# Performance work log

Measured on AMD Instinct MI355X. Metric: run time of the kernel, lower is better.

Reference implementation:

```python
import jax, jax.numpy as jnp
import numpy as np

B_BATCH = 16384   # number of independent control queries (timesteps/trials)
P = 32            # observation dim p = C.shape[0]
MC = 16           # control dim m_control = B.shape[1]
H = 24            # h (== h_tilde in the module, since it sets self.h_tilde = h)
M = 64            # m (== m_tilde, since the module sets self.m_tilde = m)
L = M + M + 1     # history length needed: max delay is j+k = m_tilde + m - 1


def setup_inputs() -> dict:
    key = jax.random.key(0)
    ks = jax.random.split(key, 9)
    return {
        # y_rev[b, d, :] == y_nat_history[-d-1] (most-recent-first reversed history)
        "y_rev": jax.random.normal(ks[0], (B_BATCH, L, P), dtype=jnp.float32),
        "M0": jax.random.normal(ks[1], (MC, P), dtype=jnp.float32),
        "M_tilde": jax.random.normal(ks[2], (H, MC, P), dtype=jnp.float32),
        "M_0l": jax.random.normal(ks[3], (H, MC, P), dtype=jnp.float32),
        "M_big": jax.random.normal(ks[4], (H, H, MC, P), dtype=jnp.float32),
        # eigenvalues of the PSD Hankel matrices: positive
        "sigma": jax.random.uniform(ks[5], (H,), dtype=jnp.float32, minval=0.01, maxval=1.0),
        "lambda_e": jax.random.uniform(ks[6], (H,), dtype=jnp.float32, minval=0.01, maxval=1.0),
        "phi": jax.random.normal(ks[7], (M, H), dtype=jnp.float32),
        "phi_tilde": jax.random.normal(ks[8], (M, H), dtype=jnp.float32),
    }


def reference(y_rev, M0, M_tilde, M_0l, M_big, sigma, lambda_e, phi, phi_tilde):
    # Term 1: M_0 @ y_t  -> [B, MC]
    u = jnp.einsum("cp,bp->bc", M0, y_rev[:, 0])

    # Term 2: sum_{i,j>=1} lambda_i^{1/4} phi_tilde[j-1,i] (M_tilde[i] @ y_{t-j})
    pt = phi_tilde * (lambda_e ** 0.25)[None, :]            # [M, H] (j-1, i)
    T2 = jnp.einsum("ji,icp->jcp", pt, M_tilde)             # [M, MC, P]
    u = u + jnp.einsum("jcp,bjp->bc", T2, y_rev[:, 1:M + 1])

    # Term 3: sum_{l,k>=0} sigma_l^{1/4} phi[k,l] (M_0l[l] @ y_{t-k})
    ps = phi * (sigma ** 0.25)[None, :]                     # [M, H] (k, l)
    T3 = jnp.einsum("kl,lcp->kcp", ps, M_0l)                # [M, MC, P]
    u = u + jnp.einsum("kcp,bkp->bc", T3, y_rev[:, 0:M])

    # Term 4: sum_{i,j,l,k} (sigma_l lambda_i)^{1/4} phi[k,l] phi_tilde[j-1,i] (M[i][l] @ y_{t-j-k})
    # Collapse (j,k) into delay d=j+k via 1-D convolution per (i,l):
    #   conv(phi_tilde[:,i], phi[:,l])[n] corresponds to delay d = n+1.
    conv = jax.vmap(jax.vmap(jnp.convolve, in_axes=(None, 1)), in_axes=(1, None))
    W4 = conv(phi_tilde, phi)                               # [H(i), H(l), 2M-1]
    scale = (lambda_e[:, None] * sigma[None, :]) ** 0.25    # [H(i), H(l)]
    T4 = jnp.einsum("ild,ilcp->dcp", W4 * scale[:, :, None], M_big)  # [2M-1, MC, P]
    u = u + jnp.einsum("dcp,bdp->bc", T4, y_rev[:, 1:2 * M])

    return u  # [B, MC]
```

## Files before the change

### kernel.cpp

```cpp
#include <hip/hip_runtime.h>
#include <hip/hip_bf16.h>

#define BB    16384
#define PP    32
#define MCC   16
#define HH    24
#define MM    64
#define LL    129
#define YROW  (LL*PP)
#define KK    (128*PP)

#define ROWS   64
#define TPB    512
#define STAGES 16
#define SK     256
#define SROWSTRIDE 265

__device__ __forceinline__ float rl(float v, int lane) {
    return __int_as_float(__builtin_amdgcn_readlane(__float_as_int(v), lane));
}

__global__ __launch_bounds__(256) void setup_k(
    const float* __restrict__ M0,  const float* __restrict__ Mt,
    const float* __restrict__ M0l, const float* __restrict__ Mb,
    const float* __restrict__ sig, const float* __restrict__ lam,
    const float* __restrict__ phi, const float* __restrict__ phit,
    float* __restrict__ Wk)
{
    __shared__ float sA[MM*HH];
    __shared__ float sB[MM*HH];
    __shared__ float sWd[HH*HH];

    const int t = threadIdx.x;
    const int d = blockIdx.x >> 1;
    const int h = blockIdx.x & 1;

#pragma unroll
    for (int r = 0; r < 6; ++r) {
        int e = t + r*256;
        int col = e % HH;
        sA[e] = phit[e] * sqrtf(sqrtf(lam[col]));
        sB[e] = phi[e]  * sqrtf(sqrtf(sig[col]));
    }
    __syncthreads();

    if (d >= 1) {
        const int n  = d - 1;
        const int lo = n > 63 ? n - 63 : 0;
        const int hi = n < 63 ? n : 63;
        for (int e = t; e < HH*HH; e += 256) {
            int i = e / HH, l = e % HH;
            float s = 0.f;
            for (int j = lo; j <= hi; ++j) s += sA[j*HH + i] * sB[(n - j)*HH + l];
            sWd[e] = s;
        }
    }
    __syncthreads();

    const int c = h*8 + (t >> 5);
    const int p = t & 31;
    float wv = 0.f;
    if (d == 0) wv += M0[c*PP + p];
    if (d >= 1 && d <= MM) {
        const int j = d - 1;
#pragma unroll
        for (int i = 0; i < HH; ++i) wv += sA[j*HH + i] * Mt[(i*MCC + c)*PP + p];
    }
    if (d < MM) {
#pragma unroll
        for (int l = 0; l < HH; ++l) wv += sB[d*HH + l] * M0l[(l*MCC + c)*PP + p];
    }
    if (d >= 1) {
        const float* mb = Mb + h*256 + t;
#pragma unroll 16
        for (int e = 0; e < HH*HH; ++e) wv += sWd[e] * mb[e*512];
    }
    Wk[(d*PP + p)*MCC + c] = wv;
}

__global__ __launch_bounds__(512) void main_k(
    const float* __restrict__ Y, const float* __restrict__ Wk,
    float* __restrict__ out)
{
    __shared__ float sY[ROWS * SROWSTRIDE];

    const int t    = threadIdx.x;
    const int w    = t >> 6;
    const int lane = t & 63;
    const int blk  = blockIdx.x;

    const int srow = t >> 3, kq = t & 7;
    const float* yst = Y + (size_t)(blk*ROWS + srow)*YROW + kq*32;
    const int wbase = srow*SROWSTRIDE + kq*33;

    const int rbase = lane*SROWSTRIDE + w*33;

    const float* wst = Wk + ((w*32 + (lane & 31))*MCC + ((lane >> 5) & 1)*8);

    float acc[16];
#pragma unroll
    for (int c = 0; c < 16; ++c) acc[c] = 0.f;

    float4 Yr[8], Wn0, Wn1, Wc0, Wc1;
#pragma unroll
    for (int i = 0; i < 8; ++i) Yr[i] = *(const float4*)(yst + 4*i);
    Wn0 = *(const float4*)(wst + 0);
    Wn1 = *(const float4*)(wst + 4);

#pragma unroll 1
    for (int s = 0; s < STAGES; ++s) {
        __syncthreads();
#pragma unroll
        for (int i = 0; i < 8; ++i) {
            int a = wbase + 4*i;
            sY[a + 0] = Yr[i].x; sY[a + 1] = Yr[i].y;
            sY[a + 2] = Yr[i].z; sY[a + 3] = Yr[i].w;
        }
        __syncthreads();

        Wc0 = Wn0; Wc1 = Wn1;
        if (s < STAGES - 1) {
            const float* yp = yst + (s + 1)*SK;
#pragma unroll
            for (int i = 0; i < 8; ++i) Yr[i] = *(const float4*)(yp + 4*i);
            const float* wp = wst + (s + 1)*SK*MCC;
            Wn0 = *(const float4*)(wp + 0);
            Wn1 = *(const float4*)(wp + 4);
        }

#pragma unroll
        for (int j = 0; j < 32; ++j) {
            float yv = sY[rbase + j];
            acc[0]  = fmaf(rl(Wc0.x, j     ), yv, acc[0]);
            acc[1]  = fmaf(rl(Wc0.y, j     ), yv, acc[1]);
            acc[2]  = fmaf(rl(Wc0.z, j     ), yv, acc[2]);
            acc[3]  = fmaf(rl(Wc0.w, j     ), yv, acc[3]);
            acc[4]  = fmaf(rl(Wc1.x, j     ), yv, acc[4]);
            acc[5]  = fmaf(rl(Wc1.y, j     ), yv, acc[5]);
            acc[6]  = fmaf(rl(Wc1.z, j     ), yv, acc[6]);
            acc[7]  = fmaf(rl(Wc1.w, j     ), yv, acc[7]);
            acc[8]  = fmaf(rl(Wc0.x, j + 32), yv, acc[8]);
            acc[9]  = fmaf(rl(Wc0.y, j + 32), yv, acc[9]);
            acc[10] = fmaf(rl(Wc0.z, j + 32), yv, acc[10]);
            acc[11] = fmaf(rl(Wc0.w, j + 32), yv, acc[11]);
            acc[12] = fmaf(rl(Wc1.x, j + 32), yv, acc[12]);
            acc[13] = fmaf(rl(Wc1.y, j + 32), yv, acc[13]);
            acc[14] = fmaf(rl(Wc1.z, j + 32), yv, acc[14]);
            acc[15] = fmaf(rl(Wc1.w, j + 32), yv, acc[15]);
        }
    }

    __syncthreads();
    float* red = sY;
#pragma unroll
    for (int c = 0; c < 16; ++c) red[t*16 + c] = acc[c];
    __syncthreads();

    if (t < 256) {
        const int row = t >> 2, c4 = t & 3;
        float4 sum = make_float4(0.f, 0.f, 0.f, 0.f);
#pragma unroll
        for (int ww = 0; ww < 8; ++ww) {
            const float* rp = &red[(ww*64 + row)*16 + c4*4];
            sum.x += rp[0]; sum.y += rp[1]; sum.z += rp[2]; sum.w += rp[3];
        }
        *(float4*)(out + (size_t)(blk*ROWS + row)*MCC + c4*4) = sum;
    }
}

extern "C" void kernel_launch(void* const* d_in, const int* in_sizes, int n_in,
                              void* d_out, int out_size, void* d_ws, size_t ws_size,
                              hipStream_t stream) {
    (void)in_sizes; (void)n_in; (void)out_size; (void)ws_size;
    const float* y    = (const float*)d_in[0];
    const float* M0   = (const float*)d_in[1];
    const float* Mt   = (const float*)d_in[2];
    const float* M0l  = (const float*)d_in[3];
    const float* Mb   = (const float*)d_in[4];
    const float* sig  = (const float*)d_in[5];
    const float* lam  = (const float*)d_in[6];
    const float* phi  = (const float*)d_in[7];
    const float* phit = (const float*)d_in[8];

    float* Wk  = (float*)d_ws;
    float* out = (float*)d_out;

    setup_k<<<256, 256, 0, stream>>>(M0, Mt, M0l, Mb, sig, lam, phi, phit, Wk);
    main_k<<<256, TPB, 0, stream>>>(y, Wk, out);
}
```

Measured before the change: 420.1 us.

## Split the K dimension across two blocks per row group and add a reduce pass

The main kernel now splits the 4096-long reduction dimension into two halves, launching 512 blocks instead of 256 so more of the GPU's compute units get work. Each half writes partial sums to the output or to a workspace buffer, and a small extra kernel adds them together. Launch bounds now request 4 blocks per multiprocessor. The cost is one extra kernel launch and an extra pass over the output, and the split path is only taken when the workspace is large enough.

```diff
diff --git a/kernel.cpp b/kernel.cpp
--- a/kernel.cpp
+++ b/kernel.cpp
@@ -9,10 +9,10 @@
 #define LL    129
 #define YROW  (LL*PP)
 #define KK    (128*PP)
+#define KHALF 2048
 
 #define ROWS   64
 #define TPB    512
-#define STAGES 16
 #define SK     256
 #define SROWSTRIDE 265
 
@@ -78,9 +78,10 @@
     Wk[(d*PP + p)*MCC + c] = wv;
 }
 
-__global__ __launch_bounds__(512) void main_k(
+template<int NSTAGES>
+__global__ __launch_bounds__(512, 4) void main_k(
     const float* __restrict__ Y, const float* __restrict__ Wk,
-    float* __restrict__ out)
+    float* __restrict__ out0, float* __restrict__ out1)
 {
     __shared__ float sY[ROWS * SROWSTRIDE];
 
@@ -88,14 +89,17 @@
     const int w    = t >> 6;
     const int lane = t & 63;
     const int blk  = blockIdx.x;
+    const int rowg = blk & 255;
+    const int kh   = blk >> 8;
 
     const int srow = t >> 3, kq = t & 7;
-    const float* yst = Y + (size_t)(blk*ROWS + srow)*YROW + kq*32;
+    const float* yst = Y + (size_t)(rowg*ROWS + srow)*YROW + kh*KHALF + kq*32;
     const int wbase = srow*SROWSTRIDE + kq*33;
 
     const int rbase = lane*SROWSTRIDE + w*33;
 
-    const float* wst = Wk + ((w*32 + (lane & 31))*MCC + ((lane >> 5) & 1)*8);
+    const float* wst = Wk + (size_t)kh*KHALF*MCC
+                         + ((w*32 + (lane & 31))*MCC + ((lane >> 5) & 1)*8);
 
     float acc[16];
 #pragma unroll
@@ -108,7 +112,7 @@
     Wn1 = *(const float4*)(wst + 4);
 
 #pragma unroll 1
-    for (int s = 0; s < STAGES; ++s) {
+    for (int s = 0; s < NSTAGES; ++s) {
         __syncthreads();
 #pragma unroll
         for (int i = 0; i < 8; ++i) {
@@ -119,7 +123,7 @@
         __syncthreads();
 
         Wc0 = Wn0; Wc1 = Wn1;
-        if (s < STAGES - 1) {
+        if (s < NSTAGES - 1) {
             const float* yp = yst + (s + 1)*SK;
 #pragma unroll
             for (int i = 0; i < 8; ++i) Yr[i] = *(const float4*)(yp + 4*i);
@@ -164,14 +168,25 @@
             const float* rp = &red[(ww*64 + row)*16 + c4*4];
             sum.x += rp[0]; sum.y += rp[1]; sum.z += rp[2]; sum.w += rp[3];
         }
-        *(float4*)(out + (size_t)(blk*ROWS + row)*MCC + c4*4) = sum;
-    }
+        float* dst = kh ? out1 : out0;
+        *(float4*)(dst + (size_t)(rowg*ROWS + row)*MCC + c4*4) = sum;
+    }
+}
+
+__global__ __launch_bounds__(256) void reduce_k(
+    const float* __restrict__ part, float* __restrict__ out)
+{
+    const int i = blockIdx.x*256 + threadIdx.x;
+    float4 a = ((float4*)out)[i];
+    float4 b = ((const float4*)part)[i];
+    a.x += b.x; a.y += b.y; a.z += b.z; a.w += b.w;
+    ((float4*)out)[i] = a;
 }
 
 extern "C" void kernel_launch(void* const* d_in, const int* in_sizes, int n_in,
                               void* d_out, int out_size, void* d_ws, size_t ws_size,
                               hipStream_t stream) {
-    (void)in_sizes; (void)n_in; (void)out_size; (void)ws_size;
+    (void)in_sizes; (void)n_in; (void)out_size;
     const float* y    = (const float*)d_in[0];
     const float* M0   = (const float*)d_in[1];
     const float* Mt   = (const float*)d_in[2];
@@ -185,6 +200,16 @@
     float* Wk  = (float*)d_ws;
     float* out = (float*)d_out;
 
+    const size_t wk_bytes   = (size_t)KK*MCC*sizeof(float);
+    const size_t part_bytes = (size_t)BB*MCC*sizeof(float);
+
     setup_k<<<256, 256, 0, stream>>>(M0, Mt, M0l, Mb, sig, lam, phi, phit, Wk);
-    main_k<<<256, TPB, 0, stream>>>(y, Wk, out);
-}
+
+    if (ws_size >= wk_bytes + part_bytes) {
+        float* part = Wk + (size_t)KK*MCC;
+        main_k<8><<<512, TPB, 0, stream>>>(y, Wk, out, part);
+        reduce_k<<<256, 256, 0, stream>>>(part, out);
+    } else {
+        main_k<16><<<256, TPB, 0, stream>>>(y, Wk, out, out);
+    }
+}
```

Result: slower. 430.6 us (+2.5%).

## Replace LDS-staged readlane GEMV with per-thread direct dot products

Applied to the files above, without the earlier changes.

The main kernel no longer stages Y through shared memory or broadcasts weights with readlane. Each thread now computes one (row, control) output as a 4096-length dot product, reading Y and a transposed weight row straight from global memory with double-buffered float4 loads. The weight layout in setup_k is transposed to be contiguous per control channel to support this. The 16 threads sharing a row re-read the same Y data through cache instead of shared memory, which removes the barriers and readlane work but raises cache and global traffic, and the final cross-warp reduction disappears.

```diff
diff --git a/kernel.cpp b/kernel.cpp
--- a/kernel.cpp
+++ b/kernel.cpp
@@ -1,5 +1,4 @@
 #include <hip/hip_runtime.h>
-#include <hip/hip_bf16.h>
 
 #define BB    16384
 #define PP    32
@@ -10,22 +9,12 @@
 #define YROW  (LL*PP)
 #define KK    (128*PP)
 
-#define ROWS   64
-#define TPB    512
-#define STAGES 16
-#define SK     256
-#define SROWSTRIDE 265
-
-__device__ __forceinline__ float rl(float v, int lane) {
-    return __int_as_float(__builtin_amdgcn_readlane(__float_as_int(v), lane));
-}
-
 __global__ __launch_bounds__(256) void setup_k(
     const float* __restrict__ M0,  const float* __restrict__ Mt,
     const float* __restrict__ M0l, const float* __restrict__ Mb,
     const float* __restrict__ sig, const float* __restrict__ lam,
     const float* __restrict__ phi, const float* __restrict__ phit,
-    float* __restrict__ Wk)
+    float* __restrict__ Wt)
 {
     __shared__ float sA[MM*HH];
     __shared__ float sB[MM*HH];
@@ -75,97 +64,47 @@
 #pragma unroll 16
         for (int e = 0; e < HH*HH; ++e) wv += sWd[e] * mb[e*512];
     }
-    Wk[(d*PP + p)*MCC + c] = wv;
+    Wt[(size_t)c*KK + d*PP + p] = wv;
 }
 
-__global__ __launch_bounds__(512) void main_k(
-    const float* __restrict__ Y, const float* __restrict__ Wk,
+#define LD(Y0,Y1,Y2,Y3,W0,W1,W2,W3,off)                                     \
+    Y0 = *(const float4*)(yp + (off));      W0 = *(const float4*)(wp + (off));      \
+    Y1 = *(const float4*)(yp + (off) + 4);  W1 = *(const float4*)(wp + (off) + 4);  \
+    Y2 = *(const float4*)(yp + (off) + 8);  W2 = *(const float4*)(wp + (off) + 8);  \
+    Y3 = *(const float4*)(yp + (off) + 12); W3 = *(const float4*)(wp + (off) + 12);
+
+#define FMA4(Yv,Wv)                                                         \
+    a0 = fmaf((Yv).x, (Wv).x, a0); a1 = fmaf((Yv).y, (Wv).y, a1);           \
+    a2 = fmaf((Yv).z, (Wv).z, a2); a3 = fmaf((Yv).w, (Wv).w, a3);
+
+__global__ __launch_bounds__(256, 4) void main_k(
+    const float* __restrict__ Y, const float* __restrict__ Wt,
     float* __restrict__ out)
 {
-    __shared__ float sY[ROWS * SROWSTRIDE];
+    const int t   = threadIdx.x;
+    const int c   = t & 15;
+    const int row = blockIdx.x * 16 + (t >> 4);
 
-    const int t    = threadIdx.x;
-    const int w    = t >> 6;
-    const int lane = t & 63;
-    const int blk  = blockIdx.x;
+    const float* yp = Y  + (size_t)row * YROW;
+    const float* wp = Wt + (size_t)c * KK;
 
-    const int srow = t >> 3, kq = t & 7;
-    const float* yst = Y + (size_t)(blk*ROWS + srow)*YROW + kq*32;
-    const int wbase = srow*SROWSTRIDE + kq*33;
+    float a0 = 0.f, a1 = 0.f, a2 = 0.f, a3 = 0.f;
+    float4 ya0, ya1, ya2, ya3, wa0, wa1, wa2, wa3;
+    float4 yb0, yb1, yb2, yb3, wb0, wb1, wb2, wb3;
 
-    const int rbase = lane*SROWSTRIDE + w*33;
-
-    const float* wst = Wk + ((w*32 + (lane & 31))*MCC + ((lane >> 5) & 1)*8);
-
-    float acc[16];
-#pragma unroll
-    for (int c = 0; c < 16; ++c) acc[c] = 0.f;
-
-    float4 Yr[8], Wn0, Wn1, Wc0, Wc1;
-#pragma unroll
-    for (int i = 0; i < 8; ++i) Yr[i] = *(const float4*)(yst + 4*i);
-    Wn0 = *(const float4*)(wst + 0);
-    Wn1 = *(const float4*)(wst + 4);
+    LD(ya0, ya1, ya2, ya3, wa0, wa1, wa2, wa3, 0)
 
 #pragma unroll 1
-    for (int s = 0; s < STAGES; ++s) {
-        __syncthreads();
-#pragma unroll
-        for (int i = 0; i < 8; ++i) {
-            int a = wbase + 4*i;
-            sY[a + 0] = Yr[i].x; sY[a + 1] = Yr[i].y;
-            sY[a + 2] = Yr[i].z; sY[a + 3] = Yr[i].w;
+    for (int q = 0; q < KK; q += 32) {
+        LD(yb0, yb1, yb2, yb3, wb0, wb1, wb2, wb3, q + 16)
+        FMA4(ya0, wa0) FMA4(ya1, wa1) FMA4(ya2, wa2) FMA4(ya3, wa3)
+        if (q + 32 < KK) {
+            LD(ya0, ya1, ya2, ya3, wa0, wa1, wa2, wa3, q + 32)
         }
-        __syncthreads();
-
-        Wc0 = Wn0; Wc1 = Wn1;
-        if (s < STAGES - 1) {
-            const float* yp = yst + (s + 1)*SK;
-#pragma unroll
-            for (int i = 0; i < 8; ++i) Yr[i] = *(const float4*)(yp + 4*i);
-            const float* wp = wst + (s + 1)*SK*MCC;
-            Wn0 = *(const float4*)(wp + 0);
-            Wn1 = *(const float4*)(wp + 4);
-        }
-
-#pragma unroll
-        for (int j = 0; j < 32; ++j) {
-            float yv = sY[rbase + j];
-            acc[0]  = fmaf(rl(Wc0.x, j     ), yv, acc[0]);
-            acc[1]  = fmaf(rl(Wc0.y, j     ), yv, acc[1]);
-            acc[2]  = fmaf(rl(Wc0.z, j     ), yv, acc[2]);
-            acc[3]  = fmaf(rl(Wc0.w, j     ), yv, acc[3]);
-            acc[4]  = fmaf(rl(Wc1.x, j     ), yv, acc[4]);
-            acc[5]  = fmaf(rl(Wc1.y, j     ), yv, acc[5]);
-            acc[6]  = fmaf(rl(Wc1.z, j     ), yv, acc[6]);
-            acc[7]  = fmaf(rl(Wc1.w, j     ), yv, acc[7]);
-            acc[8]  = fmaf(rl(Wc0.x, j + 32), yv, acc[8]);
-            acc[9]  = fmaf(rl(Wc0.y, j + 32), yv, acc[9]);
-            acc[10] = fmaf(rl(Wc0.z, j + 32), yv, acc[10]);
-            acc[11] = fmaf(rl(Wc0.w, j + 32), yv, acc[11]);
-            acc[12] = fmaf(rl(Wc1.x, j + 32), yv, acc[12]);
-            acc[13] = fmaf(rl(Wc1.y, j + 32), yv, acc[13]);
-            acc[14] = fmaf(rl(Wc1.z, j + 32), yv, acc[14]);
-            acc[15] = fmaf(rl(Wc1.w, j + 32), yv, acc[15]);
-        }
+        FMA4(yb0, wb0) FMA4(yb1, wb1) FMA4(yb2, wb2) FMA4(yb3, wb3)
     }
 
-    __syncthreads();
-    float* red = sY;
-#pragma unroll
-    for (int c = 0; c < 16; ++c) red[t*16 + c] = acc[c];
-    __syncthreads();
-
-    if (t < 256) {
-        const int row = t >> 2, c4 = t & 3;
-        float4 sum = make_float4(0.f, 0.f, 0.f, 0.f);
-#pragma unroll
-        for (int ww = 0; ww < 8; ++ww) {
-            const float* rp = &red[(ww*64 + row)*16 + c4*4];
-            sum.x += rp[0]; sum.y += rp[1]; sum.z += rp[2]; sum.w += rp[3];
-        }
-        *(float4*)(out + (size_t)(blk*ROWS + row)*MCC + c4*4) = sum;
-    }
+    out[(size_t)row * MCC + c] = (a0 + a1) + (a2 + a3);
 }
 
 extern "C" void kernel_launch(void* const* d_in, const int* in_sizes, int n_in,
@@ -182,9 +121,9 @@
     const float* phi  = (const float*)d_in[7];
     const float* phit = (const float*)d_in[8];
 
-    float* Wk  = (float*)d_ws;
+    float* Wt  = (float*)d_ws;
     float* out = (float*)d_out;
 
-    setup_k<<<256, 256, 0, stream>>>(M0, Mt, M0l, Mb, sig, lam, phi, phit, Wk);
-    main_k<<<256, TPB, 0, stream>>>(y, Wk, out);
+    setup_k<<<256, 256, 0, stream>>>(M0, Mt, M0l, Mb, sig, lam, phi, phit, Wt);
+    main_k<<<1024, 256, 0, stream>>>(y, Wt, out);
 }
```

Result: slower. 870.3 us (+107.2%).

## Double-buffer LDS tiles with XOR swizzle and halve stage size

Applied to the files above, without the earlier changes.

The main kernel now splits K into 32 stages of 128 instead of 16 stages of 256. Shared memory is double-buffered as float4 with an XOR swizzle instead of padded scalar rows, so only one barrier per stage is needed and reads are vectorized 128-bit LDS loads. The weight fragment per lane shrinks to one float4, and readlane indices are remapped to cover 16 columns per group of four. This targets barrier stalls and scalar LDS traffic, at the cost of more loop iterations and a reworked index mapping that must stay correct.

```diff
diff --git a/kernel.cpp b/kernel.cpp
--- a/kernel.cpp
+++ b/kernel.cpp
@@ -1,5 +1,4 @@
 #include <hip/hip_runtime.h>
-#include <hip/hip_bf16.h>
 
 #define BB    16384
 #define PP    32
@@ -12,9 +11,9 @@
 
 #define ROWS   64
 #define TPB    512
-#define STAGES 16
-#define SK     256
-#define SROWSTRIDE 265
+#define STAGES 32
+#define SK     128
+#define BUFF   (ROWS*SK/4)
 
 __device__ __forceinline__ float rl(float v, int lane) {
     return __int_as_float(__builtin_amdgcn_readlane(__float_as_int(v), lane));
@@ -78,11 +77,29 @@
     Wk[(d*PP + p)*MCC + c] = wv;
 }
 
+#define FMASTEP(YV, J)                                                       \
+    acc[0]  = fmaf(rl(Wc.x, (J)     ), (YV), acc[0]);                        \
+    acc[1]  = fmaf(rl(Wc.y, (J)     ), (YV), acc[1]);                        \
+    acc[2]  = fmaf(rl(Wc.z, (J)     ), (YV), acc[2]);                        \
+    acc[3]  = fmaf(rl(Wc.w, (J)     ), (YV), acc[3]);                        \
+    acc[4]  = fmaf(rl(Wc.x, (J) + 16), (YV), acc[4]);                        \
+    acc[5]  = fmaf(rl(Wc.y, (J) + 16), (YV), acc[5]);                        \
+    acc[6]  = fmaf(rl(Wc.z, (J) + 16), (YV), acc[6]);                        \
+    acc[7]  = fmaf(rl(Wc.w, (J) + 16), (YV), acc[7]);                        \
+    acc[8]  = fmaf(rl(Wc.x, (J) + 32), (YV), acc[8]);                        \
+    acc[9]  = fmaf(rl(Wc.y, (J) + 32), (YV), acc[9]);                        \
+    acc[10] = fmaf(rl(Wc.z, (J) + 32), (YV), acc[10]);                       \
+    acc[11] = fmaf(rl(Wc.w, (J) + 32), (YV), acc[11]);                       \
+    acc[12] = fmaf(rl(Wc.x, (J) + 48), (YV), acc[12]);                       \
+    acc[13] = fmaf(rl(Wc.y, (J) + 48), (YV), acc[13]);                       \
+    acc[14] = fmaf(rl(Wc.z, (J) + 48), (YV), acc[14]);                       \
+    acc[15] = fmaf(rl(Wc.w, (J) + 48), (YV), acc[15]);
+
 __global__ __launch_bounds__(512) void main_k(
     const float* __restrict__ Y, const float* __restrict__ Wk,
     float* __restrict__ out)
 {
-    __shared__ float sY[ROWS * SROWSTRIDE];
+    __shared__ float4 sY[2*BUFF];
 
     const int t    = threadIdx.x;
     const int w    = t >> 6;
@@ -90,68 +107,61 @@
     const int blk  = blockIdx.x;
 
     const int srow = t >> 3, kq = t & 7;
-    const float* yst = Y + (size_t)(blk*ROWS + srow)*YROW + kq*32;
-    const int wbase = srow*SROWSTRIDE + kq*33;
-
-    const int rbase = lane*SROWSTRIDE + w*33;
-
-    const float* wst = Wk + ((w*32 + (lane & 31))*MCC + ((lane >> 5) & 1)*8);
+    const float* yst = Y + (size_t)(blk*ROWS + srow)*YROW + kq*16;
+    const int wx = srow*32;
+    const int sx = srow & 7;
+
+    const int rbase4 = lane*32;
+    const int rx     = lane & 7;
+
+    const float* wst = Wk + ((w*16 + (lane & 15))*MCC + (lane >> 4)*4);
 
     float acc[16];
 #pragma unroll
     for (int c = 0; c < 16; ++c) acc[c] = 0.f;
 
-    float4 Yr[8], Wn0, Wn1, Wc0, Wc1;
-#pragma unroll
-    for (int i = 0; i < 8; ++i) Yr[i] = *(const float4*)(yst + 4*i);
-    Wn0 = *(const float4*)(wst + 0);
-    Wn1 = *(const float4*)(wst + 4);
+    float4 Yr[4], Wn, Wc;
+#pragma unroll
+    for (int i = 0; i < 4; ++i) Yr[i] = *(const float4*)(yst + 4*i);
+    Wn = *(const float4*)(wst);
+#pragma unroll
+    for (int i = 0; i < 4; ++i)
+        sY[wx + ((kq*4 + i) ^ sx)] = Yr[i];
 
 #pragma unroll 1
     for (int s = 0; s < STAGES; ++s) {
-        __syncthreads();
-#pragma unroll
-        for (int i = 0; i < 8; ++i) {
-            int a = wbase + 4*i;
-            sY[a + 0] = Yr[i].x; sY[a + 1] = Yr[i].y;
-            sY[a + 2] = Yr[i].z; sY[a + 3] = Yr[i].w;
-        }
-        __syncthreads();
-
-        Wc0 = Wn0; Wc1 = Wn1;
+        const int cur = s & 1;
+
+        Wc = Wn;
         if (s < STAGES - 1) {
             const float* yp = yst + (s + 1)*SK;
 #pragma unroll
-            for (int i = 0; i < 8; ++i) Yr[i] = *(const float4*)(yp + 4*i);
-            const float* wp = wst + (s + 1)*SK*MCC;
-            Wn0 = *(const float4*)(wp + 0);
-            Wn1 = *(const float4*)(wp + 4);
-        }
-
-#pragma unroll
-        for (int j = 0; j < 32; ++j) {
-            float yv = sY[rbase + j];
-            acc[0]  = fmaf(rl(Wc0.x, j     ), yv, acc[0]);
-            acc[1]  = fmaf(rl(Wc0.y, j     ), yv, acc[1]);
-            acc[2]  = fmaf(rl(Wc0.z, j     ), yv, acc[2]);
-            acc[3]  = fmaf(rl(Wc0.w, j     ), yv, acc[3]);
-            acc[4]  = fmaf(rl(Wc1.x, j     ), yv, acc[4]);
-            acc[5]  = fmaf(rl(Wc1.y, j     ), yv, acc[5]);
-            acc[6]  = fmaf(rl(Wc1.z, j     ), yv, acc[6]);
-            acc[7]  = fmaf(rl(Wc1.w, j     ), yv, acc[7]);
-            acc[8]  = fmaf(rl(Wc0.x, j + 32), yv, acc[8]);
-            acc[9]  = fmaf(rl(Wc0.y, j + 32), yv, acc[9]);
-            acc[10] = fmaf(rl(Wc0.z, j + 32), yv, acc[10]);
-            acc[11] = fmaf(rl(Wc0.w, j + 32), yv, acc[11]);
-            acc[12] = fmaf(rl(Wc1.x, j + 32), yv, acc[12]);
-            acc[13] = fmaf(rl(Wc1.y, j + 32), yv, acc[13]);
-            acc[14] = fmaf(rl(Wc1.z, j + 32), yv, acc[14]);
-            acc[15] = fmaf(rl(Wc1.w, j + 32), yv, acc[15]);
-        }
-    }
-
-    __syncthreads();
-    float* red = sY;
+            for (int i = 0; i < 4; ++i) Yr[i] = *(const float4*)(yp + 4*i);
+            Wn = *(const float4*)(wst + (size_t)(s + 1)*SK*MCC);
+        }
+
+        __syncthreads();
+
+        const float4* yb = &sY[cur*BUFF];
+#pragma unroll
+        for (int j4 = 0; j4 < 4; ++j4) {
+            float4 y4 = yb[rbase4 + ((w*4 + j4) ^ rx)];
+            FMASTEP(y4.x, j4*4 + 0)
+            FMASTEP(y4.y, j4*4 + 1)
+            FMASTEP(y4.z, j4*4 + 2)
+            FMASTEP(y4.w, j4*4 + 3)
+        }
+
+        if (s < STAGES - 1) {
+            float4* ob = &sY[(cur ^ 1)*BUFF];
+#pragma unroll
+            for (int i = 0; i < 4; ++i)
+                ob[wx + ((kq*4 + i) ^ sx)] = Yr[i];
+        }
+    }
+
+    __syncthreads();
+    float* red = (float*)sY;
 #pragma unroll
     for (int c = 0; c < 16; ++c) red[t*16 + c] = acc[c];
     __syncthreads();
```

Result: slower. 472.0 us (+12.4%).
